# Performance work log

Measured on AMD Instinct MI355X. Metric: run time of the kernel, lower is better.

The kernel has to match this reference:

```python
import jax, jax.numpy as jnp
import numpy as np

SCALE = 1.0  # alpha / rank = 32 / 32


def setup_inputs() -> dict:
    key = jax.random.key(0)
    k_x, k_w, k_b, k_a, k_bb = jax.random.split(key, 5)
    B, S, D = 4, 4096, 3072
    depth, rank = 4, 32
    x = jax.random.normal(k_x, (B, S, D), dtype=jnp.float32)
    W = jax.random.normal(k_w, (D, D), dtype=jnp.float32) * (1.0 / np.sqrt(D))
    b = jax.random.normal(k_b, (D,), dtype=jnp.float32) * 0.02
    lora_A = jax.random.normal(k_a, (depth, rank, D), dtype=jnp.float32) * (1.0 / np.sqrt(D))
    lora_B = jax.random.normal(k_bb, (depth, D, rank), dtype=jnp.float32) * 0.02
    return {"x": x, "W": W, "b": b, "lora_A": lora_A, "lora_B": lora_B}


def reference(x, W, b, lora_A, lora_B):
    # base: y = x @ W.T + b
    base_out = jnp.einsum('bsi,oi->bso', x, W) + b
    # stacked LoRA: sum_d (x @ A_d.T @ B_d.T); dropout=0 -> identity
    # down-project to rank per depth: [B,S,depth,rank]
    z = jnp.einsum('bsi,dri->bsdr', x, lora_A)
    lora_out = jnp.einsum('bsdr,dor->bso', z, lora_B)
    return base_out + lora_out * SCALE
```

## Files before the change

kernel.cpp:

```cpp
#include <hip/hip_runtime.h>
#include <hip/hip_bf16.h>


typedef unsigned short ushort_t;
typedef short bf16x8 __attribute__((ext_vector_type(8)));
typedef float floatx4 __attribute__((ext_vector_type(4)));
typedef unsigned short ushortx4 __attribute__((ext_vector_type(4)));

__device__ __forceinline__ ushort_t f2bf(float f) {
    __hip_bfloat16 h = __float2bfloat16(f);
    return *(ushort_t*)&h;
}

__device__ __forceinline__ void async_load16(const void* g, void* l) {
    __builtin_amdgcn_global_load_lds(
        (const __attribute__((address_space(1))) void*)g,
        (__attribute__((address_space(3))) void*)l,
        16, 0, 0);
}

#define MFMA16(a, b, c) __builtin_amdgcn_mfma_f32_16x16x32_bf16(a, b, c, 0, 0, 0)

__global__ __launch_bounds__(256)
void cvt_kernel(const float* __restrict__ in, ushort_t* __restrict__ out, int n4) {
    int i = blockIdx.x * 256 + threadIdx.x;
    if (i < n4) {
        const float4 v = ((const float4*)in)[i];
        ushortx4 o = { f2bf(v.x), f2bf(v.y), f2bf(v.z), f2bf(v.w) };
        ((ushortx4*)out)[i] = o;
    }
}

__global__ __launch_bounds__(256)
void transpose_loraB_kernel(const float* __restrict__ lb,
                            ushort_t* __restrict__ out) {
    int idx = blockIdx.x * 256 + threadIdx.x;
    int n = idx >> 7;
    int j = idx & 127;
    int d = j >> 5, r = j & 31;
    out[idx] = f2bf(lb[(size_t)d * (3072 * 32) + (size_t)n * 32 + r]);
}

__global__ __launch_bounds__(256)
void transpose_loraA_kernel(const float* __restrict__ la,
                            ushort_t* __restrict__ out) {
    int idx = blockIdx.x * 256 + threadIdx.x;
    int kk = idx >> 7;
    int j  = idx & 127;
    out[idx] = f2bf(la[(size_t)j * 3072 + kk]);
}

template <int KT, bool OUT_F32, bool ADD_MAT>
__global__ __launch_bounds__(256)
void gemm_bt_kernel(const ushort_t* __restrict__ A, int lda,
                    const ushort_t* __restrict__ B, int ldb,
                    const float* __restrict__ Cadd,
                    const float* __restrict__ bias,
                    void* __restrict__ Cv, int ldc)
{
    __shared__ ushort_t As[128 * 32];
    __shared__ ushort_t Bs[128 * 32];

    const int t    = threadIdx.x;
    const int lane = t & 63;
    const int wave = t >> 6;
    const int wr   = wave >> 1, wc = wave & 1;
    const int quad = lane >> 4, l16 = lane & 15;

    const int mBase = blockIdx.y * 128;
    const int nBase = blockIdx.x * 128;

    floatx4 acc[4][4] = {};

    const int p0 = t,       r0 = p0 >> 2, g0 = ((p0 & 3) ^ ((r0 >> 1) & 3)) << 3;
    const int p1 = t + 256, r1 = p1 >> 2, g1 = ((p1 & 3) ^ ((r1 >> 1) & 3)) << 3;
    const int qs = (quad ^ ((l16 >> 1) & 3)) << 3;

    for (int kt = 0; kt < KT; ++kt) {
        const int ko = kt * 32;

        async_load16(A + (size_t)(mBase + r0) * lda + ko + g0, &As[p0 * 8]);
        async_load16(A + (size_t)(mBase + r1) * lda + ko + g1, &As[p1 * 8]);
        async_load16(B + (size_t)(nBase + r0) * ldb + ko + g0, &Bs[p0 * 8]);
        async_load16(B + (size_t)(nBase + r1) * ldb + ko + g1, &Bs[p1 * 8]);

        __syncthreads();

        bf16x8 af[4], bf[4];
#pragma unroll
        for (int mi = 0; mi < 4; ++mi)
            af[mi] = *(const bf16x8*)&As[(wr * 64 + mi * 16 + l16) * 32 + qs];
#pragma unroll
        for (int ni = 0; ni < 4; ++ni)
            bf[ni] = *(const bf16x8*)&Bs[(wc * 64 + ni * 16 + l16) * 32 + qs];

#pragma unroll
        for (int mi = 0; mi < 4; ++mi)
#pragma unroll
            for (int ni = 0; ni < 4; ++ni)
                acc[mi][ni] = MFMA16(af[mi], bf[ni], acc[mi][ni]);

        __syncthreads();
    }

#pragma unroll
    for (int ni = 0; ni < 4; ++ni) {
        const int col = nBase + wc * 64 + ni * 16 + l16;
        const float bv = bias ? bias[col] : 0.0f;
#pragma unroll
        for (int mi = 0; mi < 4; ++mi) {
            const int row = mBase + wr * 64 + mi * 16 + quad * 4;
#pragma unroll
            for (int r = 0; r < 4; ++r) {
                float v = acc[mi][ni][r] + bv;
                if (ADD_MAT) v += Cadd[(size_t)(row + r) * ldc + col];
                if (OUT_F32) {
                    ((float*)Cv)[(size_t)(row + r) * ldc + col] = v;
                } else {
                    ((ushort_t*)Cv)[(size_t)(row + r) * ldc + col] = f2bf(v);
                }
            }
        }
    }
}

__global__ __launch_bounds__(512)
void gemm256_kernel(const ushort_t* __restrict__ A,
                    const ushort_t* __restrict__ B,
                    const float* __restrict__ bias,
                    float* __restrict__ C)
{
    constexpr int LDA = 3072;
    constexpr int NT  = 48;
    constexpr int NBX = 12;

    __shared__ ushort_t smem_u[65536];
    char* const smem = (char*)smem_u;

    const int t    = threadIdx.x;
    const int lane = t & 63;
    const int wave = t >> 6;
    const int wr   = wave >> 2;
    const int wc   = wave & 3;
    const int quad = lane >> 4;
    const int l16  = lane & 15;

    const int bid = blockIdx.x;
    const int sw  = (bid & 7) * 96 + (bid >> 3);
    const int bx  = sw % NBX;
    const int by  = sw / NBX;
    const int mBase = by * 256;
    const int nBase = bx * 256;

    const int prow = t >> 3;
    const int cg   = (t & 7) ^ (prow & 7);
    const ushort_t* const aSrc = A + (size_t)(mBase + prow) * LDA + cg * 8;
    const ushort_t* const bSrc = B + (size_t)(nBase + prow) * LDA + cg * 8;
    char* const aDst = smem + t * 16;
    char* const bDst = smem + 32768 + t * 16;

#define STAGE_A(c, h, kt) do {                                              \
        const ushort_t* _s = aSrc + (size_t)(h) * 128 * LDA + (kt) * 64;    \
        char* _d = aDst + (c) * 65536 + (h) * 16384;                        \
        async_load16(_s, _d);                                               \
        async_load16(_s + 64 * LDA, _d + 8192);                             \
    } while (0)
#define STAGE_B(c, h, kt) do {                                              \
        const ushort_t* _s = bSrc + (size_t)(h) * 128 * LDA + (kt) * 64;    \
        char* _d = bDst + (c) * 65536 + (h) * 16384;                        \
        async_load16(_s, _d);                                               \
        async_load16(_s + 64 * LDA, _d + 8192);                             \
    } while (0)

    const int s0  = ((0 + quad) ^ (l16 & 7)) << 4;
    const int s1  = ((4 + quad) ^ (l16 & 7)) << 4;
    const int aRd = wr * 16384 + l16 * 128;
    const int bRd = 32768 + (wc >> 1) * 16384 + ((wc & 1) * 64 + l16) * 128;

    floatx4 acc[8][4] = {};
    bf16x8 af[8][2];
    bf16x8 bfr[2][2];

    STAGE_A(0, 0, 0); STAGE_A(0, 1, 0);
    STAGE_B(0, 0, 0); STAGE_B(0, 1, 0);
    STAGE_A(1, 0, 1); STAGE_A(1, 1, 1);
    asm volatile("s_waitcnt vmcnt(4)" ::: "memory");
    __builtin_amdgcn_s_barrier();
    __builtin_amdgcn_sched_barrier(0);

    int cur = 0;
    for (int kt = 0; kt < NT; ++kt) {
        const int cb  = cur << 16;
        const int ktB = (kt + 1 < NT) ? kt + 1 : NT - 1;
        const int ktA = (kt + 2 < NT) ? kt + 2 : NT - 1;

#pragma unroll
        for (int mi = 0; mi < 4; ++mi) {
            af[mi][0] = *(const bf16x8*)(smem + cb + aRd + mi * 2048 + s0);
            af[mi][1] = *(const bf16x8*)(smem + cb + aRd + mi * 2048 + s1);
        }
#pragma unroll
        for (int nj = 0; nj < 2; ++nj) {
            bfr[nj][0] = *(const bf16x8*)(smem + cb + bRd + nj * 2048 + s0);
            bfr[nj][1] = *(const bf16x8*)(smem + cb + bRd + nj * 2048 + s1);
        }
        STAGE_B(cur ^ 1, 0, ktB);
        __builtin_amdgcn_s_barrier();
        asm volatile("s_waitcnt lgkmcnt(0)" ::: "memory");
        __builtin_amdgcn_sched_barrier(0);
        __builtin_amdgcn_s_setprio(1);
#pragma unroll
        for (int ks = 0; ks < 2; ++ks)
#pragma unroll
            for (int mi = 0; mi < 4; ++mi)
#pragma unroll
                for (int nj = 0; nj < 2; ++nj)
                    acc[mi][nj] = MFMA16(af[mi][ks], bfr[nj][ks], acc[mi][nj]);
        __builtin_amdgcn_s_setprio(0);
        __builtin_amdgcn_s_barrier();

#pragma unroll
        for (int mi = 4; mi < 8; ++mi) {
            af[mi][0] = *(const bf16x8*)(smem + cb + aRd + mi * 2048 + s0);
            af[mi][1] = *(const bf16x8*)(smem + cb + aRd + mi * 2048 + s1);
        }
        STAGE_B(cur ^ 1, 1, ktB);
        __builtin_amdgcn_s_barrier();
        asm volatile("s_waitcnt lgkmcnt(0)" ::: "memory");
        __builtin_amdgcn_sched_barrier(0);
        __builtin_amdgcn_s_setprio(1);
#pragma unroll
        for (int ks = 0; ks < 2; ++ks)
#pragma unroll
            for (int mi = 4; mi < 8; ++mi)
#pragma unroll
                for (int nj = 0; nj < 2; ++nj)
                    acc[mi][nj] = MFMA16(af[mi][ks], bfr[nj][ks], acc[mi][nj]);
        __builtin_amdgcn_s_setprio(0);
        __builtin_amdgcn_s_barrier();

#pragma unroll
        for (int nj = 0; nj < 2; ++nj) {
            bfr[nj][0] = *(const bf16x8*)(smem + cb + bRd + (2 + nj) * 2048 + s0);
            bfr[nj][1] = *(const bf16x8*)(smem + cb + bRd + (2 + nj) * 2048 + s1);
        }
        STAGE_A(cur, 0, ktA);
        __builtin_amdgcn_s_barrier();
        asm volatile("s_waitcnt lgkmcnt(0)" ::: "memory");
        __builtin_amdgcn_sched_barrier(0);
        __builtin_amdgcn_s_setprio(1);
#pragma unroll
        for (int ks = 0; ks < 2; ++ks)
#pragma unroll
            for (int mi = 0; mi < 4; ++mi)
#pragma unroll
                for (int nj = 0; nj < 2; ++nj)
                    acc[mi][2 + nj] = MFMA16(af[mi][ks], bfr[nj][ks], acc[mi][2 + nj]);
        __builtin_amdgcn_s_setprio(0);
        __builtin_amdgcn_s_barrier();

        STAGE_A(cur, 1, ktA);
        asm volatile("s_waitcnt vmcnt(4)" ::: "memory");
        __builtin_amdgcn_s_barrier();
        __builtin_amdgcn_sched_barrier(0);
        __builtin_amdgcn_s_setprio(1);
#pragma unroll
        for (int ks = 0; ks < 2; ++ks)
#pragma unroll
            for (int mi = 4; mi < 8; ++mi)
#pragma unroll
                for (int nj = 0; nj < 2; ++nj)
                    acc[mi][2 + nj] = MFMA16(af[mi][ks], bfr[nj][ks], acc[mi][2 + nj]);
        __builtin_amdgcn_s_setprio(0);
        __builtin_amdgcn_s_barrier();

        cur ^= 1;
    }

    asm volatile("s_waitcnt vmcnt(0)" ::: "memory");

#pragma unroll
    for (int ni = 0; ni < 4; ++ni) {
        const int col = nBase + wc * 64 + ni * 16 + l16;
        const float bv = bias[col];
#pragma unroll
        for (int mi = 0; mi < 8; ++mi) {
            const int row0 = mBase + wr * 128 + mi * 16 + quad * 4;
            float* cp = C + (size_t)row0 * LDA + col;
#pragma unroll
            for (int r = 0; r < 4; ++r)
                cp[(size_t)r * LDA] = acc[mi][ni][r] + bv;
        }
    }
#undef STAGE_A
#undef STAGE_B
}

extern "C" void kernel_launch(void* const* d_in, const int* in_sizes, int n_in,
                              void* d_out, int out_size, void* d_ws, size_t ws_size,
                              hipStream_t stream) {
    const float* x  = (const float*)d_in[0];
    const float* W  = (const float*)d_in[1];
    const float* b  = (const float*)d_in[2];
    const float* lA = (const float*)d_in[3];
    const float* lB = (const float*)d_in[4];
    float* out = (float*)d_out;

    constexpr int M = 4 * 4096;
    constexpr int N = 3072;
    constexpr int K = 3072;
    constexpr size_t nX  = (size_t)M * K;
    constexpr size_t nW  = (size_t)N * K;
    constexpr size_t nT  = (size_t)128 * K;

    ushort_t* xb    = (ushort_t*)d_ws;
    ushort_t* Weffb = xb + nX;
    ushort_t* Bp    = Weffb + nW;
    ushort_t* At    = Bp + nT;

    cvt_kernel<<<nX / 4 / 256, 256, 0, stream>>>(x, xb, (int)(nX / 4));

    transpose_loraB_kernel<<<nT / 256, 256, 0, stream>>>(lB, Bp);
    transpose_loraA_kernel<<<nT / 256, 256, 0, stream>>>(lA, At);

    gemm_bt_kernel<4, false, true><<<dim3(N / 128, N / 128), 256, 0, stream>>>(
        Bp, 128, At, 128, W, nullptr, Weffb, N);

    gemm256_kernel<<<(M / 256) * (N / 256), 512, 0, stream>>>(xb, Weffb, b, out);
}
```

Measured before the change: 636.6 us.

## Prefetch B two stages ahead, widen bf16 convert, merge LoRA transposes

```diff
diff --git a/kernel.cpp b/kernel.cpp
--- a/kernel.cpp
+++ b/kernel.cpp
@@ -6,6 +6,7 @@
 typedef short bf16x8 __attribute__((ext_vector_type(8)));
 typedef float floatx4 __attribute__((ext_vector_type(4)));
 typedef unsigned short ushortx4 __attribute__((ext_vector_type(4)));
+typedef unsigned short ushortx8 __attribute__((ext_vector_type(8)));
 
 __device__ __forceinline__ ushort_t f2bf(float f) {
     __hip_bfloat16 h = __float2bfloat16(f);
@@ -22,32 +23,35 @@
 #define MFMA16(a, b, c) __builtin_amdgcn_mfma_f32_16x16x32_bf16(a, b, c, 0, 0, 0)
 
 __global__ __launch_bounds__(256)
-void cvt_kernel(const float* __restrict__ in, ushort_t* __restrict__ out, int n4) {
+void cvt_kernel(const float* __restrict__ in, ushort_t* __restrict__ out, int n8) {
     int i = blockIdx.x * 256 + threadIdx.x;
-    if (i < n4) {
-        const float4 v = ((const float4*)in)[i];
-        ushortx4 o = { f2bf(v.x), f2bf(v.y), f2bf(v.z), f2bf(v.w) };
-        ((ushortx4*)out)[i] = o;
+    if (i < n8) {
+        const float4 v0 = ((const float4*)in)[2 * i];
+        const float4 v1 = ((const float4*)in)[2 * i + 1];
+        ushortx8 o = { f2bf(v0.x), f2bf(v0.y), f2bf(v0.z), f2bf(v0.w),
+                       f2bf(v1.x), f2bf(v1.y), f2bf(v1.z), f2bf(v1.w) };
+        ((ushortx8*)out)[i] = o;
     }
 }
 
 __global__ __launch_bounds__(256)
-void transpose_loraB_kernel(const float* __restrict__ lb,
-                            ushort_t* __restrict__ out) {
-    int idx = blockIdx.x * 256 + threadIdx.x;
-    int n = idx >> 7;
-    int j = idx & 127;
-    int d = j >> 5, r = j & 31;
-    out[idx] = f2bf(lb[(size_t)d * (3072 * 32) + (size_t)n * 32 + r]);
-}
-
-__global__ __launch_bounds__(256)
-void transpose_loraA_kernel(const float* __restrict__ la,
-                            ushort_t* __restrict__ out) {
-    int idx = blockIdx.x * 256 + threadIdx.x;
-    int kk = idx >> 7;
-    int j  = idx & 127;
-    out[idx] = f2bf(la[(size_t)j * 3072 + kk]);
+void transpose_lora_kernel(const float* __restrict__ lb,
+                           const float* __restrict__ la,
+                           ushort_t* __restrict__ outB,
+                           ushort_t* __restrict__ outA) {
+    int bid = blockIdx.x;
+    if (bid < 1536) {
+        int idx = bid * 256 + threadIdx.x;
+        int n = idx >> 7;
+        int j = idx & 127;
+        int d = j >> 5, r = j & 31;
+        outB[idx] = f2bf(lb[(size_t)d * (3072 * 32) + (size_t)n * 32 + r]);
+    } else {
+        int idx = (bid - 1536) * 256 + threadIdx.x;
+        int kk = idx >> 7;
+        int j  = idx & 127;
+        outA[idx] = f2bf(la[(size_t)j * 3072 + kk]);
+    }
 }
 
 template <int KT, bool OUT_F32, bool ADD_MAT>
@@ -184,14 +188,14 @@
     STAGE_A(0, 0, 0); STAGE_A(0, 1, 0);
     STAGE_B(0, 0, 0); STAGE_B(0, 1, 0);
     STAGE_A(1, 0, 1); STAGE_A(1, 1, 1);
-    asm volatile("s_waitcnt vmcnt(4)" ::: "memory");
+    STAGE_B(1, 0, 1); STAGE_B(1, 1, 1);
+    asm volatile("s_waitcnt vmcnt(8)" ::: "memory");
     __builtin_amdgcn_s_barrier();
     __builtin_amdgcn_sched_barrier(0);
 
     int cur = 0;
     for (int kt = 0; kt < NT; ++kt) {
         const int cb  = cur << 16;
-        const int ktB = (kt + 1 < NT) ? kt + 1 : NT - 1;
         const int ktA = (kt + 2 < NT) ? kt + 2 : NT - 1;
 
 #pragma unroll
@@ -204,7 +208,6 @@
             bfr[nj][0] = *(const bf16x8*)(smem + cb + bRd + nj * 2048 + s0);
             bfr[nj][1] = *(const bf16x8*)(smem + cb + bRd + nj * 2048 + s1);
         }
-        STAGE_B(cur ^ 1, 0, ktB);
         __builtin_amdgcn_s_barrier();
         asm volatile("s_waitcnt lgkmcnt(0)" ::: "memory");
         __builtin_amdgcn_sched_barrier(0);
@@ -224,7 +227,6 @@
             af[mi][0] = *(const bf16x8*)(smem + cb + aRd + mi * 2048 + s0);
             af[mi][1] = *(const bf16x8*)(smem + cb + aRd + mi * 2048 + s1);
         }
-        STAGE_B(cur ^ 1, 1, ktB);
         __builtin_amdgcn_s_barrier();
         asm volatile("s_waitcnt lgkmcnt(0)" ::: "memory");
         __builtin_amdgcn_sched_barrier(0);
@@ -245,6 +247,7 @@
             bfr[nj][1] = *(const bf16x8*)(smem + cb + bRd + (2 + nj) * 2048 + s1);
         }
         STAGE_A(cur, 0, ktA);
+        STAGE_A(cur, 1, ktA);
         __builtin_amdgcn_s_barrier();
         asm volatile("s_waitcnt lgkmcnt(0)" ::: "memory");
         __builtin_amdgcn_sched_barrier(0);
@@ -259,8 +262,8 @@
         __builtin_amdgcn_s_setprio(0);
         __builtin_amdgcn_s_barrier();
 
-        STAGE_A(cur, 1, ktA);
-        asm volatile("s_waitcnt vmcnt(4)" ::: "memory");
+        STAGE_B(cur, 0, ktA);
+        STAGE_B(cur, 1, ktA);
         __builtin_amdgcn_s_barrier();
         __builtin_amdgcn_sched_barrier(0);
         __builtin_amdgcn_s_setprio(1);
@@ -272,6 +275,8 @@
                 for (int nj = 0; nj < 2; ++nj)
                     acc[mi][2 + nj] = MFMA16(af[mi][ks], bfr[nj][ks], acc[mi][2 + nj]);
         __builtin_amdgcn_s_setprio(0);
+        __builtin_amdgcn_sched_barrier(0);
+        asm volatile("s_waitcnt vmcnt(8)" ::: "memory");
         __builtin_amdgcn_s_barrier();
 
         cur ^= 1;
@@ -318,10 +323,9 @@
     ushort_t* Bp    = Weffb + nW;
     ushort_t* At    = Bp + nT;
 
-    cvt_kernel<<<nX / 4 / 256, 256, 0, stream>>>(x, xb, (int)(nX / 4));
-
-    transpose_loraB_kernel<<<nT / 256, 256, 0, stream>>>(lB, Bp);
-    transpose_loraA_kernel<<<nT / 256, 256, 0, stream>>>(lA, At);
+    cvt_kernel<<<nX / 8 / 256, 256, 0, stream>>>(x, xb, (int)(nX / 8));
+
+    transpose_lora_kernel<<<2 * (nT / 256), 256, 0, stream>>>(lB, lA, Bp, At);
 
     gemm_bt_kernel<4, false, true><<<dim3(N / 128, N / 128), 256, 0, stream>>>(
         Bp, 128, At, 128, W, nullptr, Weffb, N);
```

New measurement: 670.8 us. +5.4%, slower.
